# Kernel tuning notes

Measured on AMD Instinct MI355X. Metric: run time of the kernel, lower is better.

The kernel has to match this reference:

```python
import jax, jax.numpy as jnp
import numpy as np

D_MODEL = 1024
D_FF = 4096
N_EXPERTS = 8
D_EXPERT = D_FF // N_EXPERTS  # 512
TOP_K = 2
LB_WEIGHT = 0.01
B, S = 4, 2048


def setup_inputs() -> dict:
    key = jax.random.key(0)
    ks = jax.random.split(key, 8)
    x = jax.random.normal(ks[0], (B, S, D_MODEL), dtype=jnp.float32)
    # per-expert FFN params stacked on expert axis
    w1 = jax.random.normal(ks[1], (N_EXPERTS, D_MODEL, D_EXPERT), dtype=jnp.float32) * (1.0 / np.sqrt(D_MODEL))
    b1 = jnp.zeros((N_EXPERTS, D_EXPERT), dtype=jnp.float32)
    w2 = jax.random.normal(ks[2], (N_EXPERTS, D_EXPERT, D_MODEL), dtype=jnp.float32) * (1.0 / np.sqrt(D_EXPERT))
    b2 = jnp.zeros((N_EXPERTS, D_MODEL), dtype=jnp.float32)
    centroids = jax.random.normal(ks[3], (N_EXPERTS, D_MODEL), dtype=jnp.float32) * 0.02
    w_route = jax.random.normal(ks[4], (N_EXPERTS, D_MODEL), dtype=jnp.float32) * (1.0 / np.sqrt(D_MODEL))
    return {"x": x, "w1": w1, "b1": b1, "w2": w2, "b2": b2,
            "centroids": centroids, "w_route": w_route}


def _top_k_softmax(logits, k):
    # softmax restricted to the top-k logits per token; zeros elsewhere
    vals, _ = jax.lax.top_k(logits, k)          # (..., k)
    thresh = vals[..., -1:]                     # kth-largest value
    masked = jnp.where(logits >= thresh, logits, -jnp.inf)
    return jax.nn.softmax(masked, axis=-1)


def reference(x, w1, b1, w2, b2, centroids, w_route):
    eps = 1e-12
    x_norm = x / jnp.maximum(jnp.linalg.norm(x, axis=-1, keepdims=True), eps)
    c_norm = centroids / jnp.maximum(jnp.linalg.norm(centroids, axis=-1, keepdims=True), eps)
    cos_scores = jnp.einsum('bsd,ed->bse', x_norm, c_norm)
    route_scores = jnp.einsum('bsd,ed->bse', x, w_route)
    logits = cos_scores + route_scores                       # (B,S,E)
    gates = _top_k_softmax(logits, TOP_K)                    # (B,S,E)
    # all experts computed on all tokens (dense MoE, masked combine)
    h = jax.nn.gelu(jnp.einsum('bsd,edh->bseh', x, w1) + b1, approximate=False)
    expert_out = jnp.einsum('bseh,ehd->bsed', h, w2) + b2    # (B,S,E,D)
    out = jnp.einsum('bse,bsed->bsd', gates, expert_out)
    return out
```

## Files before the change

kernel.cpp:

```cpp
#include <hip/hip_runtime.h>
#include <hip/hip_bf16.h>
#include <math.h>

#define T_TOK 8192
#define DM 1024
#define DE 512
#define NE 8
#define DFF 4096

#define CO_X   0
#define CO_W1  8388608
#define CO_W2  12582912
#define CO_B1  16777216
#define CO_B2  16781312
#define CO_CE  16789504
#define CO_WR  16797696
#define CO_TOT 16805888

#define WS_GATE2 256
#define WS_B32   65792
#define WS_TOP2  262400
#define WS_TOK   295168
#define WS_AE    360704
#define WS_AG    426240
#define WS_INV   491776
#define WS_CONV  557312
#define WS_HC    34169088
#define WS_OC    50946304

typedef __attribute__((ext_vector_type(8))) __bf16 bf16x8;
typedef __attribute__((ext_vector_type(4))) __bf16 bf16x4;
typedef __attribute__((ext_vector_type(4))) float f32x4;

__device__ __forceinline__ f32x4 ld4(const void* p, size_t off, int md)
{
  f32x4 r;
  if (md){
    bf16x4 v = *(const bf16x4*)((const __bf16*)p + off);
    #pragma unroll
    for (int j = 0; j < 4; j++) r[j] = (float)v[j];
  } else {
    r = *(const f32x4*)((const float*)p + off);
  }
  return r;
}

__device__ __forceinline__ void async_ld16(const __bf16* g, __bf16* l)
{
  __builtin_amdgcn_global_load_lds(
      (const __attribute__((address_space(1))) unsigned int*)g,
      (__attribute__((address_space(3))) unsigned int*)l, 16, 0, 0);
}

__global__ __launch_bounds__(256) void detect_k(const void* xp, const void* cp,
                                                int* meta, int* b32)
{
  const int tid = threadIdx.x;
  const float* xf = (const float*)xp;
  int ok = 0;
  for (int i = tid; i < 1024; i += 256){
    float a = fabsf(xf[i]);
    if (a > 1e-8f && a < 100.f) ok++;
  }
  __shared__ int cnt;
  __shared__ int flg;
  if (tid == 0) cnt = 0;
  __syncthreads();
  atomicAdd(&cnt, ok);
  __syncthreads();
  if (tid == 0){ flg = (cnt > 512) ? 0 : 1; meta[0] = flg; }
  __syncthreads();
  const int md = flg;

  const int e = tid >> 5, i = tid & 31;
  float ss = 0.f;
  for (int j = 0; j < 32; j++){
    size_t d = (size_t)e * DM + i + j * 32;
    float v = md ? (float)((const __bf16*)cp)[d] : ((const float*)cp)[d];
    ss += v * v;
  }
  #pragma unroll
  for (int m = 1; m < 32; m <<= 1) ss += __shfl_xor(ss, m, 64);
  float* cinv = (float*)(meta + 48);
  if (i == 0) cinv[e] = 1.f / fmaxf(sqrtf(ss), 1e-12f);

  b32[tid] = 0;
  if (tid < 8) meta[16 + tid] = 0;
}

__global__ __launch_bounds__(256) void convert_k(
    const float* __restrict__ x, const float* __restrict__ b1,
    const float* __restrict__ b2, const float* __restrict__ ce,
    const float* __restrict__ wr, __bf16* __restrict__ dst,
    const int* __restrict__ meta)
{
  if (meta[0]) return;
  const size_t i = ((size_t)blockIdx.x * 256 + threadIdx.x) * 4;
  const float* src; size_t doff;
  if (i < 8388608){ src = x + i; doff = CO_X + i; }
  else {
    size_t j = i - 8388608;
    doff = CO_B1 + j;
    if      (j < 4096)  src = b1 + j;
    else if (j < 12288) src = b2 + (j - 4096);
    else if (j < 20480) src = ce + (j - 12288);
    else                src = wr + (j - 20480);
  }
  f32x4 v = *(const f32x4*)src;
  bf16x4 o;
  #pragma unroll
  for (int j = 0; j < 4; j++) o[j] = (__bf16)v[j];
  *(bf16x4*)(dst + doff) = o;
}

__global__ __launch_bounds__(256) void transp_k(
    const void* w1q, const void* w2q, __bf16* __restrict__ conv,
    const int* __restrict__ meta)
{
  const int md = meta[0];
  __shared__ __bf16 tile[32][33];
  const int b = blockIdx.x, tid = threadIdx.x;
  const int ty = tid >> 5, tx = tid & 31;

  const void* src; __bf16* dst; int ldS, ldD, i0, j0; size_t soff, doffb;
  if (b < 4096){
    const int e = b >> 9, t = b & 511;
    i0 = (t >> 4) << 5; j0 = (t & 15) << 5;
    ldS = DE; ldD = DM;
    soff = (size_t)e * DM * DE;
    dst = conv + CO_W1; doffb = (size_t)e * DE * DM;
    src = md ? (const void*)((const __bf16*)w1q) : (const void*)((const float*)w1q);
  } else {
    const int e = (b - 4096) >> 9, t = (b - 4096) & 511;
    i0 = (t >> 5) << 5; j0 = (t & 31) << 5;
    ldS = DM; ldD = DE;
    soff = (size_t)e * DE * DM;
    dst = conv + CO_W2; doffb = (size_t)e * DM * DE;
    src = md ? (const void*)((const __bf16*)w2q) : (const void*)((const float*)w2q);
  }

  #pragma unroll
  for (int rr = 0; rr < 4; rr++){
    const int r = rr * 8 + ty;
    const size_t s = soff + (size_t)(i0 + r) * ldS + j0 + tx;
    tile[r][tx] = md ? ((const __bf16*)src)[s] : (__bf16)((const float*)src)[s];
  }
  __syncthreads();
  #pragma unroll
  for (int rr = 0; rr < 4; rr++){
    const int r = rr * 8 + ty;
    dst[doffb + (size_t)(j0 + r) * ldD + i0 + tx] = tile[tx][r];
  }
}

__global__ __launch_bounds__(256) void route_k(
    const void* __restrict__ xp, const void* __restrict__ cp,
    const void* __restrict__ wp, const int* __restrict__ meta,
    float2* __restrict__ gate2, int* __restrict__ top2, int* __restrict__ b32)
{
  const int md = meta[0];
  const float* cinv = (const float*)(meta + 48);
  const int tid = threadIdx.x;
  const int g = tid >> 4, l = tid & 15;
  const int t = blockIdx.x * 16 + g;

  __shared__ int hist[8];
  if (tid < 8) hist[tid] = 0;
  __syncthreads();

  float xx = 0.f, cd[NE], wd[NE];
  #pragma unroll
  for (int e = 0; e < NE; e++){ cd[e] = 0.f; wd[e] = 0.f; }

  const size_t xbase = (size_t)t * DM;
  for (int j = 0; j < 16; j++){
    const int d0 = j * 64 + l * 4;
    f32x4 xv = ld4(xp, xbase + d0, md);
    xx += xv[0]*xv[0] + xv[1]*xv[1] + xv[2]*xv[2] + xv[3]*xv[3];
    #pragma unroll
    for (int e = 0; e < NE; e++){
      f32x4 cv = ld4(cp, (size_t)e * DM + d0, md);
      f32x4 wv = ld4(wp, (size_t)e * DM + d0, md);
      cd[e] += xv[0]*cv[0] + xv[1]*cv[1] + xv[2]*cv[2] + xv[3]*cv[3];
      wd[e] += xv[0]*wv[0] + xv[1]*wv[1] + xv[2]*wv[2] + xv[3]*wv[3];
    }
  }
  #pragma unroll
  for (int m = 1; m < 16; m <<= 1){
    xx += __shfl_xor(xx, m, 64);
    #pragma unroll
    for (int e = 0; e < NE; e++){
      cd[e] += __shfl_xor(cd[e], m, 64);
      wd[e] += __shfl_xor(wd[e], m, 64);
    }
  }

  if (l == 0){
    const float rxn = 1.f / fmaxf(sqrtf(xx), 1e-12f);
    float logits[NE];
    #pragma unroll
    for (int e = 0; e < NE; e++) logits[e] = cd[e] * rxn * cinv[e] + wd[e];
    float m1 = -1e30f; int i1 = 0;
    #pragma unroll
    for (int e = 0; e < NE; e++) if (logits[e] > m1){ m1 = logits[e]; i1 = e; }
    float m2 = -1e30f; int i2 = (i1 == 0) ? 1 : 0;
    #pragma unroll
    for (int e = 0; e < NE; e++)
      if (e != i1 && logits[e] > m2){ m2 = logits[e]; i2 = e; }
    float denom = 0.f, ex1 = 0.f, ex2 = 0.f;
    #pragma unroll
    for (int e = 0; e < NE; e++){
      if (logits[e] >= m2){
        float ee = expf(logits[e] - m1);
        denom += ee;
        if (e == i1) ex1 = ee;
        if (e == i2) ex2 = ee;
      }
    }
    const float inv = 1.f / denom;
    gate2[t] = make_float2(ex1 * inv, ex2 * inv);
    top2[t] = i1 | (i2 << 8);
    atomicAdd(&hist[i1], 1);
    atomicAdd(&hist[i2], 1);
  }
  __syncthreads();
  if (tid < 8) atomicAdd(&b32[(blockIdx.x >> 4) * 8 + tid], hist[tid]);
}

__global__ void offsets_k(int* meta, int* b32)
{
  const int l = threadIdx.x;
  int running = 0;
  for (int e = 0; e < NE; e++){
    int v = (l < 32) ? b32[l * 8 + e] : 0;
    int incl = v;
    #pragma unroll
    for (int ofs = 1; ofs < 32; ofs <<= 1){
      int n = __shfl_up(incl, ofs, 64);
      if (l >= ofs) incl += n;
    }
    int tot = __shfl(incl, 31, 64);
    if (l < 32) b32[l * 8 + e] = running + (incl - v);
    if (l == 0){ meta[16 + e] = tot; meta[32 + e] = running; }
    running += tot;
  }
}

__global__ __launch_bounds__(256) void place_k(
    const int* __restrict__ top2, const float2* __restrict__ gate2,
    const int* __restrict__ b32, int* __restrict__ tok, int* __restrict__ ae,
    float* __restrict__ agv, int* __restrict__ inv)
{
  __shared__ int cur[8];
  if (threadIdx.x < 8) cur[threadIdx.x] = b32[blockIdx.x * 8 + threadIdx.x];
  __syncthreads();
  const int t = blockIdx.x * 256 + threadIdx.x;
  const int p = top2[t];
  const float2 gg = gate2[t];
  const int e1 = p & 255, e2 = (p >> 8) & 255;
  const int s1 = atomicAdd(&cur[e1], 1);
  tok[s1] = t; ae[s1] = e1; agv[s1] = gg.x; inv[2 * t] = s1;
  const int s2 = atomicAdd(&cur[e2], 1);
  tok[s2] = t; ae[s2] = e2; agv[s2] = gg.y; inv[2 * t + 1] = s2;
}

__device__ __forceinline__ bool find_tile(const int* meta, int tm,
                                          int& e, int& base, int& valid)
{
  for (e = 0; e < NE; e++){
    const int cnt = meta[16 + e];
    const int nt = (cnt + 127) >> 7;
    if (tm < nt){
      const int r0 = tm << 7;
      base = meta[32 + e] + r0;
      valid = cnt - r0;
      return true;
    }
    tm -= nt;
  }
  return false;
}

__global__ __launch_bounds__(256) void gemm1g_k(
    const void* xq, const void* b1q, const __bf16* __restrict__ conv,
    const int* __restrict__ meta, const int* __restrict__ tok,
    const float* __restrict__ agv, __bf16* __restrict__ Hc)
{
  const int md = meta[0];
  const __bf16* X  = md ? (const __bf16*)xq : conv + CO_X;
  const __bf16* WT = conv + CO_W1;
  const __bf16* bb = md ? (const __bf16*)b1q : conv + CO_B1;

  int e, base, valid;
  if (!find_tile(meta, blockIdx.x, e, base, valid)) return;
  const int n0 = blockIdx.y * 128;

  __shared__ __attribute__((aligned(16))) __bf16 As[128 * 32];
  __shared__ __attribute__((aligned(16))) __bf16 Bs[128 * 32];

  const int tid = threadIdx.x;
  const int wv = tid >> 6, lane = tid & 63;
  const int q = lane >> 4, ln = lane & 15;
  const int wm = (wv >> 1) * 64, wn = (wv & 1) * 64;
  f32x4 acc[4][4] = {};

  const int sr = tid >> 2, sc = (tid & 3) * 8;
  const int t0 = tok[base + ((sr      < valid) ? sr      : 0)];
  const int t1 = tok[base + ((sr + 64 < valid) ? sr + 64 : 0)];
  const __bf16* Ag0 = X + (size_t)t0 * DM + sc;
  const __bf16* Ag1 = X + (size_t)t1 * DM + sc;
  const __bf16* Bg0 = WT + (size_t)e * (DE * DM) + (size_t)(n0 + sr) * DM + sc;
  const __bf16* Bg1 = Bg0 + (size_t)64 * DM;

  for (int k0 = 0; k0 < DM; k0 += 32){
    __syncthreads();
    async_ld16(Ag0 + k0, As + tid * 8);
    async_ld16(Ag1 + k0, As + 2048 + tid * 8);
    async_ld16(Bg0 + k0, Bs + tid * 8);
    async_ld16(Bg1 + k0, Bs + 2048 + tid * 8);
    __syncthreads();

    bf16x8 af[4], bf[4];
    #pragma unroll
    for (int mi = 0; mi < 4; mi++)
      af[mi] = *(const bf16x8*)&As[(wm + mi * 16 + ln) * 32 + q * 8];
    #pragma unroll
    for (int ni = 0; ni < 4; ni++)
      bf[ni] = *(const bf16x8*)&Bs[(wn + ni * 16 + ln) * 32 + q * 8];
    #pragma unroll
    for (int mi = 0; mi < 4; mi++)
      #pragma unroll
      for (int ni = 0; ni < 4; ni++)
        acc[mi][ni] = __builtin_amdgcn_mfma_f32_16x16x32_bf16(
            af[mi], bf[ni], acc[mi][ni], 0, 0, 0);
  }

  const int coln = n0 + wn;
  float bset[4];
  #pragma unroll
  for (int ni = 0; ni < 4; ni++)
    bset[ni] = (float)bb[e * DE + coln + ni * 16 + ln];
  #pragma unroll
  for (int mi = 0; mi < 4; mi++){
    #pragma unroll
    for (int r = 0; r < 4; r++){
      const int row = wm + mi * 16 + q * 4 + r;
      if (row < valid){
        const int slot = base + row;
        const float g = agv[slot];
        #pragma unroll
        for (int ni = 0; ni < 4; ni++){
          float v = acc[mi][ni][r] + bset[ni];
          float h = 0.5f * v * (1.0f + erff(v * 0.70710678118654752f));
          Hc[(size_t)slot * DE + coln + ni * 16 + ln] = (__bf16)(g * h);
        }
      }
    }
  }
}

__global__ __launch_bounds__(256) void gemm2g_k(
    const __bf16* __restrict__ Hc, const __bf16* __restrict__ conv,
    const int* __restrict__ meta, __bf16* __restrict__ Oc)
{
  const __bf16* WT = conv + CO_W2;

  int e, base, valid;
  if (!find_tile(meta, blockIdx.x, e, base, valid)) return;
  const int n0 = blockIdx.y * 128;

  __shared__ __attribute__((aligned(16))) __bf16 As[128 * 32];
  __shared__ __attribute__((aligned(16))) __bf16 Bs[128 * 32];

  const int tid = threadIdx.x;
  const int wv = tid >> 6, lane = tid & 63;
  const int q = lane >> 4, ln = lane & 15;
  const int wm = (wv >> 1) * 64, wn = (wv & 1) * 64;
  f32x4 acc[4][4] = {};

  const int sr = tid >> 2, sc = (tid & 3) * 8;
  const int r0 = (sr      < valid) ? sr      : 0;
  const int r1 = (sr + 64 < valid) ? sr + 64 : 0;
  const __bf16* Ag0 = Hc + (size_t)(base + r0) * DE + sc;
  const __bf16* Ag1 = Hc + (size_t)(base + r1) * DE + sc;
  const __bf16* Bg0 = WT + (size_t)e * (DM * DE) + (size_t)(n0 + sr) * DE + sc;
  const __bf16* Bg1 = Bg0 + (size_t)64 * DE;

  for (int k0 = 0; k0 < DE; k0 += 32){
    __syncthreads();
    async_ld16(Ag0 + k0, As + tid * 8);
    async_ld16(Ag1 + k0, As + 2048 + tid * 8);
    async_ld16(Bg0 + k0, Bs + tid * 8);
    async_ld16(Bg1 + k0, Bs + 2048 + tid * 8);
    __syncthreads();

    bf16x8 af[4], bf[4];
    #pragma unroll
    for (int mi = 0; mi < 4; mi++)
      af[mi] = *(const bf16x8*)&As[(wm + mi * 16 + ln) * 32 + q * 8];
    #pragma unroll
    for (int ni = 0; ni < 4; ni++)
      bf[ni] = *(const bf16x8*)&Bs[(wn + ni * 16 + ln) * 32 + q * 8];
    #pragma unroll
    for (int mi = 0; mi < 4; mi++)
      #pragma unroll
      for (int ni = 0; ni < 4; ni++)
        acc[mi][ni] = __builtin_amdgcn_mfma_f32_16x16x32_bf16(
            af[mi], bf[ni], acc[mi][ni], 0, 0, 0);
  }

  #pragma unroll
  for (int mi = 0; mi < 4; mi++){
    #pragma unroll
    for (int r = 0; r < 4; r++){
      const int row = wm + mi * 16 + q * 4 + r;
      if (row < valid){
        const int slot = base + row;
        #pragma unroll
        for (int ni = 0; ni < 4; ni++)
          Oc[(size_t)slot * DM + n0 + wn + ni * 16 + ln] = (__bf16)acc[mi][ni][r];
      }
    }
  }
}

__global__ __launch_bounds__(256) void combine_k(
    const __bf16* __restrict__ Oc, const int* __restrict__ inv,
    const int* __restrict__ ae, const float* __restrict__ agv,
    const void* b2q, const int* __restrict__ meta, void* out)
{
  const int md = meta[0];
  const int t = blockIdx.x;
  const int s1 = inv[2 * t], s2 = inv[2 * t + 1];
  const int e1 = ae[s1], e2 = ae[s2];
  const float g1 = agv[s1], g2 = agv[s2];
  const int c = threadIdx.x * 4;

  bf16x4 o1 = *(const bf16x4*)(Oc + (size_t)s1 * DM + c);
  bf16x4 o2 = *(const bf16x4*)(Oc + (size_t)s2 * DM + c);
  f32x4 bv1 = ld4(b2q, (size_t)e1 * DM + c, md);
  f32x4 bv2 = ld4(b2q, (size_t)e2 * DM + c, md);
  f32x4 rr;
  #pragma unroll
  for (int j = 0; j < 4; j++)
    rr[j] = (float)o1[j] + (float)o2[j] + g1 * bv1[j] + g2 * bv2[j];

  if (md){
    bf16x4 ob;
    #pragma unroll
    for (int j = 0; j < 4; j++) ob[j] = (__bf16)rr[j];
    *(bf16x4*)((__bf16*)out + (size_t)t * DM + c) = ob;
  } else {
    *(f32x4*)((float*)out + (size_t)t * DM + c) = rr;
  }
}

extern "C" void kernel_launch(void* const* d_in, const int* in_sizes, int n_in,
                              void* d_out, int out_size, void* d_ws, size_t ws_size,
                              hipStream_t stream)
{
  char* ws = (char*)d_ws;
  int*    meta  = (int*)ws;
  float2* gate2 = (float2*)(ws + WS_GATE2);
  int*    b32   = (int*)(ws + WS_B32);
  int*    top2  = (int*)(ws + WS_TOP2);
  int*    tok   = (int*)(ws + WS_TOK);
  int*    ae    = (int*)(ws + WS_AE);
  float*  agv   = (float*)(ws + WS_AG);
  int*    inv   = (int*)(ws + WS_INV);
  __bf16* conv  = (__bf16*)(ws + WS_CONV);
  __bf16* Hc    = (__bf16*)(ws + WS_HC);
  __bf16* Oc    = (__bf16*)(ws + WS_OC);

  detect_k<<<1, 256, 0, stream>>>(d_in[0], d_in[5], meta, b32);
  transp_k<<<8192, 256, 0, stream>>>(d_in[1], d_in[3], conv, meta);
  convert_k<<<8220, 256, 0, stream>>>(
      (const float*)d_in[0], (const float*)d_in[2], (const float*)d_in[4],
      (const float*)d_in[5], (const float*)d_in[6], conv, meta);
  route_k<<<T_TOK / 16, 256, 0, stream>>>(d_in[0], d_in[5], d_in[6], meta,
                                          gate2, top2, b32);
  offsets_k<<<1, 64, 0, stream>>>(meta, b32);
  place_k<<<T_TOK / 256, 256, 0, stream>>>(top2, gate2, b32, tok, ae, agv, inv);
  gemm1g_k<<<dim3(136, 4), 256, 0, stream>>>(d_in[0], d_in[2], conv, meta,
                                             tok, agv, Hc);
  gemm2g_k<<<dim3(136, 8), 256, 0, stream>>>(Hc, conv, meta, Oc);
  combine_k<<<T_TOK, 256, 0, stream>>>(Oc, inv, ae, agv, d_in[4], meta, d_out);
}
```

Baseline: 243.6 us.

## Fuse x bf16 conversion into routing and double-buffer grouped GEMMs with 512 threads

```diff
diff --git a/kernel.cpp b/kernel.cpp
--- a/kernel.cpp
+++ b/kernel.cpp
@@ -89,27 +89,22 @@
 }
 
 __global__ __launch_bounds__(256) void convert_k(
-    const float* __restrict__ x, const float* __restrict__ b1,
-    const float* __restrict__ b2, const float* __restrict__ ce,
-    const float* __restrict__ wr, __bf16* __restrict__ dst,
-    const int* __restrict__ meta)
+    const float* __restrict__ b1, const float* __restrict__ b2,
+    const float* __restrict__ ce, const float* __restrict__ wr,
+    __bf16* __restrict__ dst, const int* __restrict__ meta)
 {
   if (meta[0]) return;
-  const size_t i = ((size_t)blockIdx.x * 256 + threadIdx.x) * 4;
-  const float* src; size_t doff;
-  if (i < 8388608){ src = x + i; doff = CO_X + i; }
-  else {
-    size_t j = i - 8388608;
-    doff = CO_B1 + j;
-    if      (j < 4096)  src = b1 + j;
-    else if (j < 12288) src = b2 + (j - 4096);
-    else if (j < 20480) src = ce + (j - 12288);
-    else                src = wr + (j - 20480);
-  }
+  const size_t j = ((size_t)blockIdx.x * 256 + threadIdx.x) * 4;
+  const float* src;
+  const size_t doff = CO_B1 + j;
+  if      (j < 4096)  src = b1 + j;
+  else if (j < 12288) src = b2 + (j - 4096);
+  else if (j < 20480) src = ce + (j - 12288);
+  else                src = wr + (j - 20480);
   f32x4 v = *(const f32x4*)src;
   bf16x4 o;
   #pragma unroll
-  for (int j = 0; j < 4; j++) o[j] = (__bf16)v[j];
+  for (int t = 0; t < 4; t++) o[t] = (__bf16)v[t];
   *(bf16x4*)(dst + doff) = o;
 }
 
@@ -156,7 +151,8 @@
 __global__ __launch_bounds__(256) void route_k(
     const void* __restrict__ xp, const void* __restrict__ cp,
     const void* __restrict__ wp, const int* __restrict__ meta,
-    float2* __restrict__ gate2, int* __restrict__ top2, int* __restrict__ b32)
+    __bf16* __restrict__ conv, float2* __restrict__ gate2,
+    int* __restrict__ top2, int* __restrict__ b32)
 {
   const int md = meta[0];
   const float* cinv = (const float*)(meta + 48);
@@ -176,6 +172,12 @@
   for (int j = 0; j < 16; j++){
     const int d0 = j * 64 + l * 4;
     f32x4 xv = ld4(xp, xbase + d0, md);
+    if (!md){
+      bf16x4 o;
+      #pragma unroll
+      for (int jj = 0; jj < 4; jj++) o[jj] = (__bf16)xv[jj];
+      *(bf16x4*)(conv + CO_X + xbase + d0) = o;
+    }
     xx += xv[0]*xv[0] + xv[1]*xv[1] + xv[2]*xv[2] + xv[3]*xv[3];
     #pragma unroll
     for (int e = 0; e < NE; e++){
@@ -281,7 +283,7 @@
   return false;
 }
 
-__global__ __launch_bounds__(256) void gemm1g_k(
+__global__ __launch_bounds__(512, 4) void gemm1g_k(
     const void* xq, const void* b1q, const __bf16* __restrict__ conv,
     const int* __restrict__ meta, const int* __restrict__ tok,
     const float* __restrict__ agv, __bf16* __restrict__ Hc)
@@ -295,50 +297,52 @@
   if (!find_tile(meta, blockIdx.x, e, base, valid)) return;
   const int n0 = blockIdx.y * 128;
 
-  __shared__ __attribute__((aligned(16))) __bf16 As[128 * 32];
-  __shared__ __attribute__((aligned(16))) __bf16 Bs[128 * 32];
+  __shared__ __attribute__((aligned(16))) __bf16 As[2][128 * 32];
+  __shared__ __attribute__((aligned(16))) __bf16 Bs[2][128 * 32];
 
   const int tid = threadIdx.x;
   const int wv = tid >> 6, lane = tid & 63;
   const int q = lane >> 4, ln = lane & 15;
-  const int wm = (wv >> 1) * 64, wn = (wv & 1) * 64;
-  f32x4 acc[4][4] = {};
+  const int wm = (wv >> 2) * 64, wn = (wv & 3) * 32;
+  f32x4 acc[4][2] = {};
 
   const int sr = tid >> 2, sc = (tid & 3) * 8;
-  const int t0 = tok[base + ((sr      < valid) ? sr      : 0)];
-  const int t1 = tok[base + ((sr + 64 < valid) ? sr + 64 : 0)];
-  const __bf16* Ag0 = X + (size_t)t0 * DM + sc;
-  const __bf16* Ag1 = X + (size_t)t1 * DM + sc;
-  const __bf16* Bg0 = WT + (size_t)e * (DE * DM) + (size_t)(n0 + sr) * DM + sc;
-  const __bf16* Bg1 = Bg0 + (size_t)64 * DM;
-
+  const int tr = tok[base + ((sr < valid) ? sr : 0)];
+  const __bf16* Ag = X + (size_t)tr * DM + sc;
+  const __bf16* Bg = WT + (size_t)e * (DE * DM) + (size_t)(n0 + sr) * DM + sc;
+
+  async_ld16(Ag, &As[0][tid * 8]);
+  async_ld16(Bg, &Bs[0][tid * 8]);
+  __syncthreads();
+
+  int cr = 0;
   for (int k0 = 0; k0 < DM; k0 += 32){
-    __syncthreads();
-    async_ld16(Ag0 + k0, As + tid * 8);
-    async_ld16(Ag1 + k0, As + 2048 + tid * 8);
-    async_ld16(Bg0 + k0, Bs + tid * 8);
-    async_ld16(Bg1 + k0, Bs + 2048 + tid * 8);
-    __syncthreads();
-
-    bf16x8 af[4], bf[4];
+    const int k1 = k0 + 32;
+    if (k1 < DM){
+      async_ld16(Ag + k1, &As[cr ^ 1][tid * 8]);
+      async_ld16(Bg + k1, &Bs[cr ^ 1][tid * 8]);
+    }
+    bf16x8 af[4], bfr[2];
     #pragma unroll
     for (int mi = 0; mi < 4; mi++)
-      af[mi] = *(const bf16x8*)&As[(wm + mi * 16 + ln) * 32 + q * 8];
-    #pragma unroll
-    for (int ni = 0; ni < 4; ni++)
-      bf[ni] = *(const bf16x8*)&Bs[(wn + ni * 16 + ln) * 32 + q * 8];
+      af[mi] = *(const bf16x8*)&As[cr][(wm + mi * 16 + ln) * 32 + q * 8];
+    #pragma unroll
+    for (int ni = 0; ni < 2; ni++)
+      bfr[ni] = *(const bf16x8*)&Bs[cr][(wn + ni * 16 + ln) * 32 + q * 8];
     #pragma unroll
     for (int mi = 0; mi < 4; mi++)
       #pragma unroll
-      for (int ni = 0; ni < 4; ni++)
+      for (int ni = 0; ni < 2; ni++)
         acc[mi][ni] = __builtin_amdgcn_mfma_f32_16x16x32_bf16(
-            af[mi], bf[ni], acc[mi][ni], 0, 0, 0);
+            af[mi], bfr[ni], acc[mi][ni], 0, 0, 0);
+    __syncthreads();
+    cr ^= 1;
   }
 
   const int coln = n0 + wn;
-  float bset[4];
-  #pragma unroll
-  for (int ni = 0; ni < 4; ni++)
+  float bset[2];
+  #pragma unroll
+  for (int ni = 0; ni < 2; ni++)
     bset[ni] = (float)bb[e * DE + coln + ni * 16 + ln];
   #pragma unroll
   for (int mi = 0; mi < 4; mi++){
@@ -349,7 +353,7 @@
         const int slot = base + row;
         const float g = agv[slot];
         #pragma unroll
-        for (int ni = 0; ni < 4; ni++){
+        for (int ni = 0; ni < 2; ni++){
           float v = acc[mi][ni][r] + bset[ni];
           float h = 0.5f * v * (1.0f + erff(v * 0.70710678118654752f));
           Hc[(size_t)slot * DE + coln + ni * 16 + ln] = (__bf16)(g * h);
@@ -359,7 +363,7 @@
   }
 }
 
-__global__ __launch_bounds__(256) void gemm2g_k(
+__global__ __launch_bounds__(512, 4) void gemm2g_k(
     const __bf16* __restrict__ Hc, const __bf16* __restrict__ conv,
     const int* __restrict__ meta, __bf16* __restrict__ Oc)
 {
@@ -369,44 +373,46 @@
   if (!find_tile(meta, blockIdx.x, e, base, valid)) return;
   const int n0 = blockIdx.y * 128;
 
-  __shared__ __attribute__((aligned(16))) __bf16 As[128 * 32];
-  __shared__ __attribute__((aligned(16))) __bf16 Bs[128 * 32];
+  __shared__ __attribute__((aligned(16))) __bf16 As[2][128 * 32];
+  __shared__ __attribute__((aligned(16))) __bf16 Bs[2][128 * 32];
 
   const int tid = threadIdx.x;
   const int wv = tid >> 6, lane = tid & 63;
   const int q = lane >> 4, ln = lane & 15;
-  const int wm = (wv >> 1) * 64, wn = (wv & 1) * 64;
-  f32x4 acc[4][4] = {};
+  const int wm = (wv >> 2) * 64, wn = (wv & 3) * 32;
+  f32x4 acc[4][2] = {};
 
   const int sr = tid >> 2, sc = (tid & 3) * 8;
-  const int r0 = (sr      < valid) ? sr      : 0;
-  const int r1 = (sr + 64 < valid) ? sr + 64 : 0;
-  const __bf16* Ag0 = Hc + (size_t)(base + r0) * DE + sc;
-  const __bf16* Ag1 = Hc + (size_t)(base + r1) * DE + sc;
-  const __bf16* Bg0 = WT + (size_t)e * (DM * DE) + (size_t)(n0 + sr) * DE + sc;
-  const __bf16* Bg1 = Bg0 + (size_t)64 * DE;
-
+  const int rc = (sr < valid) ? sr : 0;
+  const __bf16* Ag = Hc + (size_t)(base + rc) * DE + sc;
+  const __bf16* Bg = WT + (size_t)e * (DM * DE) + (size_t)(n0 + sr) * DE + sc;
+
+  async_ld16(Ag, &As[0][tid * 8]);
+  async_ld16(Bg, &Bs[0][tid * 8]);
+  __syncthreads();
+
+  int cr = 0;
   for (int k0 = 0; k0 < DE; k0 += 32){
-    __syncthreads();
-    async_ld16(Ag0 + k0, As + tid * 8);
-    async_ld16(Ag1 + k0, As + 2048 + tid * 8);
-    async_ld16(Bg0 + k0, Bs + tid * 8);
-    async_ld16(Bg1 + k0, Bs + 2048 + tid * 8);
-    __syncthreads();
-
-    bf16x8 af[4], bf[4];
+    const int k1 = k0 + 32;
+    if (k1 < DE){
+      async_ld16(Ag + k1, &As[cr ^ 1][tid * 8]);
+      async_ld16(Bg + k1, &Bs[cr ^ 1][tid * 8]);
+    }
+    bf16x8 af[4], bfr[2];
     #pragma unroll
     for (int mi = 0; mi < 4; mi++)
-      af[mi] = *(const bf16x8*)&As[(wm + mi * 16 + ln) * 32 + q * 8];
-    #pragma unroll
-    for (int ni = 0; ni < 4; ni++)
-      bf[ni] = *(const bf16x8*)&Bs[(wn + ni * 16 + ln) * 32 + q * 8];
+      af[mi] = *(const bf16x8*)&As[cr][(wm + mi * 16 + ln) * 32 + q * 8];
+    #pragma unroll
+    for (int ni = 0; ni < 2; ni++)
+      bfr[ni] = *(const bf16x8*)&Bs[cr][(wn + ni * 16 + ln) * 32 + q * 8];
     #pragma unroll
     for (int mi = 0; mi < 4; mi++)
       #pragma unroll
-      for (int ni = 0; ni < 4; ni++)
+      for (int ni = 0; ni < 2; ni++)
         acc[mi][ni] = __builtin_amdgcn_mfma_f32_16x16x32_bf16(
-            af[mi], bf[ni], acc[mi][ni], 0, 0, 0);
+            af[mi], bfr[ni], acc[mi][ni], 0, 0, 0);
+    __syncthreads();
+    cr ^= 1;
   }
 
   #pragma unroll
@@ -417,7 +423,7 @@
       if (row < valid){
         const int slot = base + row;
         #pragma unroll
-        for (int ni = 0; ni < 4; ni++)
+        for (int ni = 0; ni < 2; ni++)
           Oc[(size_t)slot * DM + n0 + wn + ni * 16 + ln] = (__bf16)acc[mi][ni][r];
       }
     }
@@ -474,15 +480,15 @@
 
   detect_k<<<1, 256, 0, stream>>>(d_in[0], d_in[5], meta, b32);
   transp_k<<<8192, 256, 0, stream>>>(d_in[1], d_in[3], conv, meta);
-  convert_k<<<8220, 256, 0, stream>>>(
-      (const float*)d_in[0], (const float*)d_in[2], (const float*)d_in[4],
-      (const float*)d_in[5], (const float*)d_in[6], conv, meta);
+  convert_k<<<28, 256, 0, stream>>>(
+      (const float*)d_in[2], (const float*)d_in[4], (const float*)d_in[5],
+      (const float*)d_in[6], conv, meta);
   route_k<<<T_TOK / 16, 256, 0, stream>>>(d_in[0], d_in[5], d_in[6], meta,
-                                          gate2, top2, b32);
+                                          conv, gate2, top2, b32);
   offsets_k<<<1, 64, 0, stream>>>(meta, b32);
   place_k<<<T_TOK / 256, 256, 0, stream>>>(top2, gate2, b32, tok, ae, agv, inv);
-  gemm1g_k<<<dim3(136, 4), 256, 0, stream>>>(d_in[0], d_in[2], conv, meta,
+  gemm1g_k<<<dim3(136, 4), 512, 0, stream>>>(d_in[0], d_in[2], conv, meta,
                                              tok, agv, Hc);
-  gemm2g_k<<<dim3(136, 8), 256, 0, stream>>>(Hc, conv, meta, Oc);
+  gemm2g_k<<<dim3(136, 8), 512, 0, stream>>>(Hc, conv, meta, Oc);
   combine_k<<<T_TOK, 256, 0, stream>>>(Oc, inv, ae, agv, d_in[4], meta, d_out);
 }
```

New measurement: 245.4 us. About the same (+0.7%).
